# Performance work log

Hardware: AMD Instinct MI355X
Metric: run time of the kernel (lower is better)

## Reference

```python
import jax, jax.numpy as jnp
import numpy as np

N_NODES = 100000
N_EDGES = 3200000
D = 64        # z feature dim
NHID = 2 * D  # lin1 in/out features


def setup_inputs() -> dict:
    key = jax.random.key(0)
    k = jax.random.split(key, 6)
    z = jax.random.normal(k[0], (N_NODES, D), dtype=jnp.float32)
    row = jax.random.randint(k[1], (N_EDGES,), 0, N_NODES)
    col = jax.random.randint(k[2], (N_EDGES,), 0, N_NODES)
    # Kaiming-ish scale for readability; exact init is irrelevant for correctness
    W1 = jax.random.normal(k[3], (NHID, NHID), dtype=jnp.float32) / np.sqrt(NHID)
    b1 = jnp.zeros((NHID,), dtype=jnp.float32)
    W2 = jax.random.normal(k[4], (1, NHID), dtype=jnp.float32) / np.sqrt(NHID)
    b2 = jnp.zeros((1,), dtype=jnp.float32)
    return {"z": z, "row": row, "col": col, "W1": W1, "b1": b1, "W2": W2, "b2": b2}


def reference(z, row, col, W1, b1, W2, b2):
    # Gather endpoint embeddings and concat -> [E, 2D]
    e = jnp.concatenate([z[row], z[col]], axis=-1)
    h = jax.nn.relu(e @ W1.T + b1)          # [E, NHID]
    out = h @ W2.T + b2                      # [E, 1]
    return out.reshape(-1)
```

## Files before the change

kernel.cpp:

```cpp
#include <hip/hip_runtime.h>
#include <stdint.h>


typedef __attribute__((ext_vector_type(8))) short bf16x8;
typedef __attribute__((ext_vector_type(4))) float f32x4;

__device__ inline unsigned short f2bf(float f) {
    uint32_t u = __builtin_bit_cast(uint32_t, f);
    uint32_t r = (u + 0x7FFFu + ((u >> 16) & 1u)) >> 16;
    return (unsigned short)r;
}

__global__ __launch_bounds__(256) void node_precompute_mfma(
    const float* __restrict__ z, const float* __restrict__ W1,
    const float* __restrict__ b1, unsigned short* __restrict__ UV,
    int n_nodes)
{
    __shared__ __align__(16) unsigned short zs[16][72];

    const int tid = threadIdx.x;
    const int w  = tid >> 6;
    const int l  = tid & 63;
    const int lm = l & 15;
    const int q  = l >> 4;

    bf16x8 bfrag[4][2];
    float  bias[4];
#pragma unroll
    for (int nt = 0; nt < 4; ++nt) {
        const int n = w * 64 + nt * 16 + lm;
        const float* wrow = (n < 128) ? (W1 + (size_t)n * 128)
                                      : (W1 + (size_t)(n - 128) * 128 + 64);
#pragma unroll
        for (int kh = 0; kh < 2; ++kh) {
            const int k0 = kh * 32 + q * 8;
            bf16x8 bb;
#pragma unroll
            for (int j = 0; j < 8; ++j) bb[j] = (short)f2bf(wrow[k0 + j]);
            bfrag[nt][kh] = bb;
        }
        bias[nt] = (n < 128) ? b1[n] : 0.f;
    }

    const int ntiles = (n_nodes + 15) >> 4;
    const int iters = (ntiles + gridDim.x - 1) / gridDim.x;
    int tile = blockIdx.x;

    const int srow = tid >> 4;
    const int scol = (tid & 15) * 4;

    for (int it = 0; it < iters; ++it, tile += gridDim.x) {
        const int node0 = tile * 16;
        if (tile < ntiles) {
            float4 zv = make_float4(0.f, 0.f, 0.f, 0.f);
            if (node0 + srow < n_nodes)
                zv = *(const float4*)(z + (size_t)(node0 + srow) * 64 + scol);
            unsigned short* p = &zs[srow][scol];
            p[0] = f2bf(zv.x); p[1] = f2bf(zv.y); p[2] = f2bf(zv.z); p[3] = f2bf(zv.w);
        }
        __syncthreads();
        if (tile < ntiles) {
            bf16x8 afrag[2];
#pragma unroll
            for (int kh = 0; kh < 2; ++kh)
                afrag[kh] = *(const bf16x8*)&zs[lm][kh * 32 + q * 8];

            f32x4 acc[4];
#pragma unroll
            for (int nt = 0; nt < 4; ++nt) acc[nt] = (f32x4){0.f, 0.f, 0.f, 0.f};
#pragma unroll
            for (int kh = 0; kh < 2; ++kh)
#pragma unroll
                for (int nt = 0; nt < 4; ++nt)
                    acc[nt] = __builtin_amdgcn_mfma_f32_16x16x32_bf16(
                        afrag[kh], bfrag[nt][kh], acc[nt], 0, 0, 0);

#pragma unroll
            for (int nt = 0; nt < 4; ++nt) {
                const int ncol = w * 64 + nt * 16 + lm;
#pragma unroll
                for (int r = 0; r < 4; ++r) {
                    const int node = node0 + q * 4 + r;
                    if (node < n_nodes)
                        UV[(size_t)node * 256 + ncol] = f2bf(acc[nt][r] + bias[nt]);
                }
            }
        }
        __syncthreads();
    }
}

__device__ inline float acc2(uint32_t u, uint32_t v, float w0, float w1, float s) {
    float ul = __builtin_bit_cast(float, u << 16);
    float uh = __builtin_bit_cast(float, u & 0xFFFF0000u);
    float vl = __builtin_bit_cast(float, v << 16);
    float vh = __builtin_bit_cast(float, v & 0xFFFF0000u);
    s = fmaf(fmaxf(ul + vl, 0.f), w0, s);
    s = fmaf(fmaxf(uh + vh, 0.f), w1, s);
    return s;
}

__global__ __launch_bounds__(256) void edge_kernel(
    const unsigned short* __restrict__ UV,
    const int* __restrict__ row, const int* __restrict__ col,
    const float* __restrict__ W2, const float* __restrict__ b2,
    float* __restrict__ out, int E)
{
    const int sub = threadIdx.x & 15;
    const float4 w2a = *(const float4*)&W2[sub * 8];
    const float4 w2b = *(const float4*)&W2[sub * 8 + 4];
    const float bb = b2[0];

    int g = blockIdx.x * 16 + (threadIdx.x >> 4);
    const int stride = gridDim.x * 16;

    for (; g < E; g += stride) {
        const int r = row[g];
        const int c = col[g];
        uint4 uu = *(const uint4*)(UV + (size_t)r * 256 + sub * 8);
        uint4 vv = *(const uint4*)(UV + (size_t)c * 256 + 128 + sub * 8);
        float s = 0.f;
        s = acc2(uu.x, vv.x, w2a.x, w2a.y, s);
        s = acc2(uu.y, vv.y, w2a.z, w2a.w, s);
        s = acc2(uu.z, vv.z, w2b.x, w2b.y, s);
        s = acc2(uu.w, vv.w, w2b.z, w2b.w, s);
        s += __shfl_xor(s, 1, 16);
        s += __shfl_xor(s, 2, 16);
        s += __shfl_xor(s, 4, 16);
        s += __shfl_xor(s, 8, 16);
        if (sub == 0) out[g] = s + bb;
    }
}

extern "C" void kernel_launch(void* const* d_in, const int* in_sizes, int n_in,
                              void* d_out, int out_size, void* d_ws, size_t ws_size,
                              hipStream_t stream) {
    const float* z   = (const float*)d_in[0];
    const int*   row = (const int*)d_in[1];
    const int*   col = (const int*)d_in[2];
    const float* W1  = (const float*)d_in[3];
    const float* b1  = (const float*)d_in[4];
    const float* W2  = (const float*)d_in[5];
    const float* b2  = (const float*)d_in[6];
    float* out = (float*)d_out;

    const int n_nodes = in_sizes[0] / 64;
    const int E = in_sizes[1];

    unsigned short* UV = (unsigned short*)d_ws;

    node_precompute_mfma<<<512, 256, 0, stream>>>(z, W1, b1, UV, n_nodes);

    edge_kernel<<<4096, 256, 0, stream>>>(UV, row, col, W2, b2, out, E);
}
```

Measured before the change: 326.8 us.

## Swap MFMA operands in node precompute to drop LDS staging and vectorize stores

The node projection kernel now puts the weights in the A operand and z in the B operand, so each lane loads its node's z row straight from global memory into registers. This removes the shared-memory tile and both block barriers. The transposed accumulator layout lets each lane write four consecutive bf16 outputs as one 8-byte store instead of scattered 2-byte stores, and the weight and bias loads are vectorized. The grid is raised to up to 1024 blocks. The edge kernel, which likely dominates the runtime, is unchanged.

```diff
diff --git a/kernel.cpp b/kernel.cpp
--- a/kernel.cpp
+++ b/kernel.cpp
@@ -11,82 +11,85 @@
     return (unsigned short)r;
 }
 
+__device__ inline bf16x8 pack8(float4 a, float4 b) {
+    bf16x8 o;
+    o[0] = (short)f2bf(a.x); o[1] = (short)f2bf(a.y);
+    o[2] = (short)f2bf(a.z); o[3] = (short)f2bf(a.w);
+    o[4] = (short)f2bf(b.x); o[5] = (short)f2bf(b.y);
+    o[6] = (short)f2bf(b.z); o[7] = (short)f2bf(b.w);
+    return o;
+}
+
 __global__ __launch_bounds__(256) void node_precompute_mfma(
     const float* __restrict__ z, const float* __restrict__ W1,
     const float* __restrict__ b1, unsigned short* __restrict__ UV,
     int n_nodes)
 {
-    __shared__ __align__(16) unsigned short zs[16][72];
-
     const int tid = threadIdx.x;
     const int w  = tid >> 6;
     const int l  = tid & 63;
     const int lm = l & 15;
     const int q  = l >> 4;
 
-    bf16x8 bfrag[4][2];
-    float  bias[4];
+    bf16x8 wfrag[4][2];
+    float4 bias[4];
 #pragma unroll
     for (int nt = 0; nt < 4; ++nt) {
-        const int n = w * 64 + nt * 16 + lm;
-        const float* wrow = (n < 128) ? (W1 + (size_t)n * 128)
-                                      : (W1 + (size_t)(n - 128) * 128 + 64);
+        const int c = w * 64 + nt * 16 + lm;
+        const float* wrow = (c < 128) ? (W1 + (size_t)c * 128)
+                                      : (W1 + (size_t)(c - 128) * 128 + 64);
 #pragma unroll
         for (int kh = 0; kh < 2; ++kh) {
             const int k0 = kh * 32 + q * 8;
-            bf16x8 bb;
-#pragma unroll
-            for (int j = 0; j < 8; ++j) bb[j] = (short)f2bf(wrow[k0 + j]);
-            bfrag[nt][kh] = bb;
+            float4 w0 = *(const float4*)(wrow + k0);
+            float4 w1 = *(const float4*)(wrow + k0 + 4);
+            wfrag[nt][kh] = pack8(w0, w1);
         }
-        bias[nt] = (n < 128) ? b1[n] : 0.f;
+        const int cb = w * 64 + nt * 16 + q * 4;
+        bias[nt] = (cb < 128) ? *(const float4*)&b1[cb]
+                              : make_float4(0.f, 0.f, 0.f, 0.f);
     }
 
     const int ntiles = (n_nodes + 15) >> 4;
-    const int iters = (ntiles + gridDim.x - 1) / gridDim.x;
-    int tile = blockIdx.x;
 
-    const int srow = tid >> 4;
-    const int scol = (tid & 15) * 4;
+    for (int tile = blockIdx.x; tile < ntiles; tile += gridDim.x) {
+        const int node = tile * 16 + lm;
+        bf16x8 zfrag[2];
+        if (node < n_nodes) {
+            const float* zp = z + (size_t)node * 64;
+#pragma unroll
+            for (int kh = 0; kh < 2; ++kh) {
+                float4 z0 = *(const float4*)(zp + kh * 32 + q * 8);
+                float4 z1 = *(const float4*)(zp + kh * 32 + q * 8 + 4);
+                zfrag[kh] = pack8(z0, z1);
+            }
+        } else {
+            zfrag[0] = (bf16x8){0,0,0,0,0,0,0,0};
+            zfrag[1] = (bf16x8){0,0,0,0,0,0,0,0};
+        }
 
-    for (int it = 0; it < iters; ++it, tile += gridDim.x) {
-        const int node0 = tile * 16;
-        if (tile < ntiles) {
-            float4 zv = make_float4(0.f, 0.f, 0.f, 0.f);
-            if (node0 + srow < n_nodes)
-                zv = *(const float4*)(z + (size_t)(node0 + srow) * 64 + scol);
-            unsigned short* p = &zs[srow][scol];
-            p[0] = f2bf(zv.x); p[1] = f2bf(zv.y); p[2] = f2bf(zv.z); p[3] = f2bf(zv.w);
-        }
-        __syncthreads();
-        if (tile < ntiles) {
-            bf16x8 afrag[2];
+        f32x4 acc[4];
 #pragma unroll
-            for (int kh = 0; kh < 2; ++kh)
-                afrag[kh] = *(const bf16x8*)&zs[lm][kh * 32 + q * 8];
+        for (int nt = 0; nt < 4; ++nt) acc[nt] = (f32x4){0.f, 0.f, 0.f, 0.f};
+#pragma unroll
+        for (int kh = 0; kh < 2; ++kh)
+#pragma unroll
+            for (int nt = 0; nt < 4; ++nt)
+                acc[nt] = __builtin_amdgcn_mfma_f32_16x16x32_bf16(
+                    wfrag[nt][kh], zfrag[kh], acc[nt], 0, 0, 0);
 
-            f32x4 acc[4];
-#pragma unroll
-            for (int nt = 0; nt < 4; ++nt) acc[nt] = (f32x4){0.f, 0.f, 0.f, 0.f};
-#pragma unroll
-            for (int kh = 0; kh < 2; ++kh)
-#pragma unroll
-                for (int nt = 0; nt < 4; ++nt)
-                    acc[nt] = __builtin_amdgcn_mfma_f32_16x16x32_bf16(
-                        afrag[kh], bfrag[nt][kh], acc[nt], 0, 0, 0);
-
+        if (node < n_nodes) {
+            unsigned short* up = UV + (size_t)node * 256;
 #pragma unroll
             for (int nt = 0; nt < 4; ++nt) {
-                const int ncol = w * 64 + nt * 16 + lm;
-#pragma unroll
-                for (int r = 0; r < 4; ++r) {
-                    const int node = node0 + q * 4 + r;
-                    if (node < n_nodes)
-                        UV[(size_t)node * 256 + ncol] = f2bf(acc[nt][r] + bias[nt]);
-                }
+                uint2 p;
+                p.x = (uint32_t)f2bf(acc[nt][0] + bias[nt].x)
+                    | ((uint32_t)f2bf(acc[nt][1] + bias[nt].y) << 16);
+                p.y = (uint32_t)f2bf(acc[nt][2] + bias[nt].z)
+                    | ((uint32_t)f2bf(acc[nt][3] + bias[nt].w) << 16);
+                *(uint2*)(up + w * 64 + nt * 16 + q * 4) = p;
             }
         }
-        __syncthreads();
     }
 }
 
@@ -149,7 +152,9 @@
 
     unsigned short* UV = (unsigned short*)d_ws;
 
-    node_precompute_mfma<<<512, 256, 0, stream>>>(z, W1, b1, UV, n_nodes);
+    const int ntiles = (n_nodes + 15) >> 4;
+    const int nblocks = (ntiles < 1024) ? ntiles : 1024;
+    node_precompute_mfma<<<nblocks, 256, 0, stream>>>(z, W1, b1, UV, n_nodes);
 
     edge_kernel<<<4096, 256, 0, stream>>>(UV, row, col, W2, b2, out, E);
 }
```

After: 330.1 us. About the same (+1.0%).
